# Kernel optimization log

Hardware: AMD Instinct MI355X
Metric: run time of the kernel (lower is better)

## Reference

```python
import jax, jax.numpy as jnp
import numpy as np

NUM_EMBEDDINGS = 8192
EMB_CHANNELS = 8
BETA = 0.25


def setup_inputs() -> dict:
    key = jax.random.key(0)
    k1, k2 = jax.random.split(key)
    z = jax.random.normal(k1, (8, EMB_CHANNELS, 64, 64), dtype=jnp.float32)
    # torch init: uniform(-1/K, 1/K)
    lim = 1.0 / NUM_EMBEDDINGS
    codebook = jax.random.uniform(
        k2, (NUM_EMBEDDINGS, EMB_CHANNELS), dtype=jnp.float32,
        minval=-lim, maxval=lim)
    return {"z": z, "codebook": codebook}


def reference(z, codebook):
    # z: [B, C, H, W]; codebook: [K, C]
    C = codebook.shape[1]
    z_ch = jnp.moveaxis(z, 1, -1)                 # [B, H, W, C]
    z_flat = z_ch.reshape(-1, C)                  # [N, C]
    # squared-euclidean distances via sum-of-squares + matmul: [N, K]
    dist = (
        jnp.sum(z_flat ** 2, axis=1, keepdims=True)
        + jnp.sum(codebook ** 2, axis=1)
        - 2.0 * jnp.einsum('nd,kd->nk', z_flat, codebook)
    )
    idx = jnp.argmin(dist, axis=1)                # [N]
    z_q = codebook[idx].reshape(z_ch.shape)       # [B, H, W, C]
    z_q = jnp.moveaxis(z_q, -1, 1)                # [B, C, H, W]
    sg = jax.lax.stop_gradient
    loss = (BETA * jnp.mean((sg(z_q) - z) ** 2)
            + jnp.mean((z_q - sg(z)) ** 2))
    # straight-through estimator
    z_q_st = z + sg(z_q - z)
    return z_q_st, loss
```

## Files before the change

kernel.cpp:

```cpp
#include <hip/hip_runtime.h>

typedef __attribute__((ext_vector_type(8))) short short8;
typedef __attribute__((ext_vector_type(4))) float f32x4;

#define NROWS 32768
#define NELEM 262144
#define KCB   8192

static __device__ __forceinline__ short to_bf16(float x) {
    unsigned u = __float_as_uint(x);
    unsigned r = (u + 0x7FFFu + ((u >> 16) & 1u)) >> 16;
    return (short)r;
}

__global__ __launch_bounds__(256) void vq_prep(
    const float* __restrict__ z, const float* __restrict__ cb,
    short8* __restrict__ cbb, short8* __restrict__ pka, float* __restrict__ out)
{
    int gid = blockIdx.x * 256 + threadIdx.x;
    if (gid == 0) out[NELEM] = 0.0f;
    if (gid < KCB) {
        const float4* p = (const float4*)(cb + (size_t)gid * 8);
        float4 a = p[0], b = p[1];
        float h = -0.5f * (a.x*a.x + a.y*a.y + a.z*a.z + a.w*a.w
                         + b.x*b.x + b.y*b.y + b.z*b.z + b.w*b.w);
        short8 lo = { to_bf16(a.x), to_bf16(a.y), to_bf16(a.z), to_bf16(a.w),
                      to_bf16(b.x), to_bf16(b.y), to_bf16(b.z), to_bf16(b.w) };
        short8 hi = { to_bf16(h), 0, 0, 0, 0, 0, 0, 0 };
        cbb[2 * gid]     = lo;
        cbb[2 * gid + 1] = hi;
    } else {
        int n = gid - KCB;
        int bb = n >> 12, hw = n & 4095;
        const float* zp = z + (size_t)bb * 32768 + hw;
        short8 v = { to_bf16(zp[0]),     to_bf16(zp[4096]),
                     to_bf16(zp[8192]),  to_bf16(zp[12288]),
                     to_bf16(zp[16384]), to_bf16(zp[20480]),
                     to_bf16(zp[24576]), to_bf16(zp[28672]) };
        pka[n] = v;
    }
}

__global__ __launch_bounds__(512, 4) void vq_main(
    const float* __restrict__ z, const float* __restrict__ cb,
    const short8* __restrict__ cbb, const short8* __restrict__ pka,
    float* __restrict__ out)
{
    __shared__ float sbest[8][64];
    __shared__ float lsum[8];

    const int tid  = threadIdx.x;
    const int lane = tid & 63;
    const int w    = tid >> 6;
    const int col  = lane & 15;
    const int g    = lane >> 4;

    const int row0 = blockIdx.x * 64;

    short8 af[4];
    #pragma unroll
    for (int f = 0; f < 4; ++f) {
        short8 v = {0, 0, 0, 0, 0, 0, 0, 0};
        if (g == 0)      v = pka[row0 + f * 16 + col];
        else if (g == 1) v[0] = (short)0x3F80;
        af[f] = v;
    }

    const int kbase = w * 1024;
    const char* bp = (const char*)cbb + (size_t)(kbase + col) * 32
                                      + (size_t)(g & 1) * 16;

    float best[4][4];
    #pragma unroll
    for (int f = 0; f < 4; ++f)
        #pragma unroll
        for (int r = 0; r < 4; ++r)
            best[f][r] = __uint_as_float(0xFF800000u);

    const unsigned inv0 = (unsigned)(8191 - (kbase + col));
    const f32x4 zacc = {0.f, 0.f, 0.f, 0.f};

    #pragma unroll 4
    for (int t = 0; t < 64; ++t) {
        short8 bf = *(const short8*)(bp + (size_t)t * 512);
        unsigned iv = inv0 - (unsigned)(t * 16);
        #pragma unroll
        for (int f = 0; f < 4; ++f) {
            f32x4 acc = __builtin_amdgcn_mfma_f32_16x16x32_bf16(af[f], bf, zacc, 0, 0, 0);
            #pragma unroll
            for (int r = 0; r < 4; ++r) {
                float p = __uint_as_float((__float_as_uint(acc[r]) & 0xFFFFE000u) | iv);
                best[f][r] = fmaxf(best[f][r], p);
            }
        }
    }

    #pragma unroll
    for (int d = 1; d < 16; d <<= 1)
        #pragma unroll
        for (int f = 0; f < 4; ++f)
            #pragma unroll
            for (int r = 0; r < 4; ++r)
                best[f][r] = fmaxf(best[f][r], __shfl_xor(best[f][r], d));

    if (col == 0) {
        #pragma unroll
        for (int f = 0; f < 4; ++f)
            #pragma unroll
            for (int r = 0; r < 4; ++r)
                sbest[w][f * 16 + g * 4 + r] = best[f][r];
    }
    __syncthreads();

    const int pos = tid & 63;
    const int ch  = tid >> 6;
    float m = sbest[0][pos];
    #pragma unroll
    for (int kw = 1; kw < 8; ++kw) m = fmaxf(m, sbest[kw][pos]);
    const int k = 8191 - (int)(__float_as_uint(m) & 8191u);

    const int n = row0 + pos;
    const size_t o = ((size_t)(n >> 12)) * 32768 + (size_t)ch * 4096 + (size_t)(n & 4095);
    float ev = cb[(size_t)k * 8 + ch];
    float zz = z[o];
    out[o] = ev;
    float dd = ev - zz;
    float sq = dd * dd;
    #pragma unroll
    for (int off = 32; off > 0; off >>= 1) sq += __shfl_down(sq, off);
    if (lane == 0) lsum[w] = sq;
    __syncthreads();
    if (tid == 0) {
        float s = lsum[0] + lsum[1] + lsum[2] + lsum[3]
                + lsum[4] + lsum[5] + lsum[6] + lsum[7];
        atomicAdd(out + NELEM, s * (1.25f / (float)NELEM));
    }
}

extern "C" void kernel_launch(void* const* d_in, const int* in_sizes, int n_in,
                              void* d_out, int out_size, void* d_ws, size_t ws_size,
                              hipStream_t stream)
{
    const float* z  = (const float*)d_in[0];
    const float* cb = (const float*)d_in[1];
    float* out = (float*)d_out;
    short8* cbb = (short8*)d_ws;
    short8* pka = (short8*)((char*)d_ws + 256 * 1024);

    vq_prep<<<(KCB + NROWS) / 256, 256, 0, stream>>>(z, cb, cbb, pka, out);
    vq_main<<<NROWS / 64, 512, 0, stream>>>(z, cb, cbb, pka, out);
}
```

Measured before the change: 33.61 us.

## Double rows per block with 16 waves and software-prefetch codebook tiles

Each block now handles 128 rows with 1024 threads (16 waves), and each wave covers 512 codebook entries instead of 1024. Every wave keeps 8 row fragments, so each loaded codebook tile feeds twice as many MFMAs, which halves total codebook reads. The inner loop is fully unrolled with explicit double-buffered prefetch of the next two tiles. In exchange, register pressure rises (8x4 best values plus 8 A fragments), and the grid halves to 256 blocks, which may reduce occupancy.

```diff
diff --git a/kernel.cpp b/kernel.cpp
--- a/kernel.cpp
+++ b/kernel.cpp
@@ -6,6 +6,8 @@
 #define NROWS 32768
 #define NELEM 262144
 #define KCB   8192
+#define ROWS_PB 128
+#define NWAVE 16
 
 static __device__ __forceinline__ short to_bf16(float x) {
     unsigned u = __float_as_uint(x);
@@ -41,13 +43,13 @@
     }
 }
 
-__global__ __launch_bounds__(512, 4) void vq_main(
+__global__ __launch_bounds__(1024, 4) void vq_main(
     const float* __restrict__ z, const float* __restrict__ cb,
     const short8* __restrict__ cbb, const short8* __restrict__ pka,
     float* __restrict__ out)
 {
-    __shared__ float sbest[8][64];
-    __shared__ float lsum[8];
+    __shared__ float sbest[NWAVE][ROWS_PB];
+    __shared__ float lsum[NWAVE];
 
     const int tid  = threadIdx.x;
     const int lane = tid & 63;
@@ -55,24 +57,24 @@
     const int col  = lane & 15;
     const int g    = lane >> 4;
 
-    const int row0 = blockIdx.x * 64;
+    const int row0 = blockIdx.x * ROWS_PB;
 
-    short8 af[4];
+    short8 af[8];
     #pragma unroll
-    for (int f = 0; f < 4; ++f) {
+    for (int f = 0; f < 8; ++f) {
         short8 v = {0, 0, 0, 0, 0, 0, 0, 0};
         if (g == 0)      v = pka[row0 + f * 16 + col];
         else if (g == 1) v[0] = (short)0x3F80;
         af[f] = v;
     }
 
-    const int kbase = w * 1024;
-    const char* bp = (const char*)cbb + (size_t)(kbase + col) * 32
-                                      + (size_t)(g & 1) * 16;
+    const int kbase = w * (KCB / NWAVE);
+    const char* bpc = (const char*)cbb + (size_t)(kbase + col) * 32
+                                       + (size_t)(g & 1) * 16;
 
-    float best[4][4];
+    float best[8][4];
     #pragma unroll
-    for (int f = 0; f < 4; ++f)
+    for (int f = 0; f < 8; ++f)
         #pragma unroll
         for (int r = 0; r < 4; ++r)
             best[f][r] = __uint_as_float(0xFF800000u);
@@ -80,12 +82,12 @@
     const unsigned inv0 = (unsigned)(8191 - (kbase + col));
     const f32x4 zacc = {0.f, 0.f, 0.f, 0.f};
 
-    #pragma unroll 4
-    for (int t = 0; t < 64; ++t) {
-        short8 bf = *(const short8*)(bp + (size_t)t * 512);
+#define LDT(T) (*(const short8*)(bpc + (size_t)(T) * 512))
+
+    auto comp = [&](short8 bf, int t) {
         unsigned iv = inv0 - (unsigned)(t * 16);
         #pragma unroll
-        for (int f = 0; f < 4; ++f) {
+        for (int f = 0; f < 8; ++f) {
             f32x4 acc = __builtin_amdgcn_mfma_f32_16x16x32_bf16(af[f], bf, zacc, 0, 0, 0);
             #pragma unroll
             for (int r = 0; r < 4; ++r) {
@@ -93,30 +95,41 @@
                 best[f][r] = fmaxf(best[f][r], p);
             }
         }
+    };
+
+    short8 c0 = LDT(0);
+    short8 c1 = LDT(1);
+    #pragma unroll
+    for (int tt = 0; tt < 16; ++tt) {
+        short8 n0, n1;
+        if (tt < 15) { n0 = LDT(2 * tt + 2); n1 = LDT(2 * tt + 3); }
+        comp(c0, 2 * tt);
+        comp(c1, 2 * tt + 1);
+        if (tt < 15) { c0 = n0; c1 = n1; }
     }
 
     #pragma unroll
     for (int d = 1; d < 16; d <<= 1)
         #pragma unroll
-        for (int f = 0; f < 4; ++f)
+        for (int f = 0; f < 8; ++f)
             #pragma unroll
             for (int r = 0; r < 4; ++r)
                 best[f][r] = fmaxf(best[f][r], __shfl_xor(best[f][r], d));
 
     if (col == 0) {
         #pragma unroll
-        for (int f = 0; f < 4; ++f)
+        for (int f = 0; f < 8; ++f)
             #pragma unroll
             for (int r = 0; r < 4; ++r)
                 sbest[w][f * 16 + g * 4 + r] = best[f][r];
     }
     __syncthreads();
 
-    const int pos = tid & 63;
-    const int ch  = tid >> 6;
+    const int pos = tid & 127;
+    const int ch  = tid >> 7;
     float m = sbest[0][pos];
     #pragma unroll
-    for (int kw = 1; kw < 8; ++kw) m = fmaxf(m, sbest[kw][pos]);
+    for (int kw = 1; kw < NWAVE; ++kw) m = fmaxf(m, sbest[kw][pos]);
     const int k = 8191 - (int)(__float_as_uint(m) & 8191u);
 
     const int n = row0 + pos;
@@ -131,8 +144,9 @@
     if (lane == 0) lsum[w] = sq;
     __syncthreads();
     if (tid == 0) {
-        float s = lsum[0] + lsum[1] + lsum[2] + lsum[3]
-                + lsum[4] + lsum[5] + lsum[6] + lsum[7];
+        float s = 0.f;
+        #pragma unroll
+        for (int kw = 0; kw < NWAVE; ++kw) s += lsum[kw];
         atomicAdd(out + NELEM, s * (1.25f / (float)NELEM));
     }
 }
@@ -148,5 +162,5 @@
     short8* pka = (short8*)((char*)d_ws + 256 * 1024);
 
     vq_prep<<<(KCB + NROWS) / 256, 256, 0, stream>>>(z, cb, cbb, pka, out);
-    vq_main<<<NROWS / 64, 512, 0, stream>>>(z, cb, cbb, pka, out);
+    vq_main<<<NROWS / ROWS_PB, 1024, 0, stream>>>(z, cb, cbb, pka, out);
 }
```

Result: slower. 39.48 us (+17.5%).

## Stream codebook tiles into per-wave LDS ring via async global_load_lds

Applied to the files above, without the earlier changes.

Replaces the direct per-iteration global loads of bf16 codebook fragments with a 4-deep per-wave LDS ring filled by global_load_lds, using vmcnt waits to overlap loading with MFMA work. Each step now processes two 16-code tiles, and the source addresses are XOR-swizzled to avoid LDS bank conflicts when reading fragments back. Launch bounds are raised to request 6 blocks per CU. This is meant to hide global memory latency in the distance loop, at the cost of extra LDS usage, LDS read traffic and more register pressure under the tighter occupancy target.

```diff
diff --git a/kernel.cpp b/kernel.cpp
--- a/kernel.cpp
+++ b/kernel.cpp
@@ -6,6 +6,8 @@
 #define NROWS 32768
 #define NELEM 262144
 #define KCB   8192
+#define ROWS_PB 64
+#define RING  4
 
 static __device__ __forceinline__ short to_bf16(float x) {
     unsigned u = __float_as_uint(x);
@@ -41,13 +43,16 @@
     }
 }
 
-__global__ __launch_bounds__(512, 4) void vq_main(
+#define WAITVM(n) asm volatile("s_waitcnt vmcnt(" #n ")" ::: "memory")
+
+__global__ __launch_bounds__(512, 6) void vq_main(
     const float* __restrict__ z, const float* __restrict__ cb,
     const short8* __restrict__ cbb, const short8* __restrict__ pka,
     float* __restrict__ out)
 {
-    __shared__ float sbest[8][64];
-    __shared__ float lsum[8];
+    __shared__ short8 ring[8][RING][64];
+    __shared__ float  sbest[8][ROWS_PB];
+    __shared__ float  lsum[8];
 
     const int tid  = threadIdx.x;
     const int lane = tid & 63;
@@ -55,7 +60,7 @@
     const int col  = lane & 15;
     const int g    = lane >> 4;
 
-    const int row0 = blockIdx.x * 64;
+    const int row0 = blockIdx.x * ROWS_PB;
 
     short8 af[4];
     #pragma unroll
@@ -67,8 +72,9 @@
     }
 
     const int kbase = w * 1024;
-    const char* bp = (const char*)cbb + (size_t)(kbase + col) * 32
-                                      + (size_t)(g & 1) * 16;
+    const char* cbbase = (const char*)cbb + (size_t)kbase * 32;
+    const unsigned srcswz = ((unsigned)lane * 16u) ^ (((unsigned)lane & 8u) << 1);
+    const int boff = col * 32 + (((g & 1) ^ ((col >> 2) & 1)) << 4);
 
     float best[4][4];
     #pragma unroll
@@ -80,20 +86,40 @@
     const unsigned inv0 = (unsigned)(8191 - (kbase + col));
     const f32x4 zacc = {0.f, 0.f, 0.f, 0.f};
 
-    #pragma unroll 4
-    for (int t = 0; t < 64; ++t) {
-        short8 bf = *(const short8*)(bp + (size_t)t * 512);
-        unsigned iv = inv0 - (unsigned)(t * 16);
+#define STAGE(p) __builtin_amdgcn_global_load_lds( \
+        (const __attribute__((address_space(1))) void*)(cbbase + (size_t)(p) * 1024 + srcswz), \
+        (__attribute__((address_space(3))) void*)&ring[w][(p) & 3][0], 16, 0, 0)
+
+    asm volatile("s_waitcnt vmcnt(0)" ::: "memory");
+    STAGE(0); STAGE(1); STAGE(2); STAGE(3);
+
+    auto comp2 = [&](const short8* base, unsigned iv0) {
+        short8 b0 = *(const short8*)((const char*)base + boff);
+        short8 b1 = *(const short8*)((const char*)base + boff + 512);
+        unsigned iv1 = iv0 - 16u;
         #pragma unroll
         for (int f = 0; f < 4; ++f) {
-            f32x4 acc = __builtin_amdgcn_mfma_f32_16x16x32_bf16(af[f], bf, zacc, 0, 0, 0);
+            f32x4 a0 = __builtin_amdgcn_mfma_f32_16x16x32_bf16(af[f], b0, zacc, 0, 0, 0);
+            f32x4 a1 = __builtin_amdgcn_mfma_f32_16x16x32_bf16(af[f], b1, zacc, 0, 0, 0);
             #pragma unroll
             for (int r = 0; r < 4; ++r) {
-                float p = __uint_as_float((__float_as_uint(acc[r]) & 0xFFFFE000u) | iv);
-                best[f][r] = fmaxf(best[f][r], p);
+                float p0 = __uint_as_float((__float_as_uint(a0[r]) & 0xFFFFE000u) | iv0);
+                float p1 = __uint_as_float((__float_as_uint(a1[r]) & 0xFFFFE000u) | iv1);
+                best[f][r] = fmaxf(fmaxf(p0, p1), best[f][r]);
             }
         }
+    };
+
+    #pragma unroll 4
+    for (int p = 0; p < 28; ++p) {
+        WAITVM(3);
+        comp2(&ring[w][p & 3][0], inv0 - (unsigned)(p * 32));
+        STAGE(p + 4);
     }
+    WAITVM(3); comp2(&ring[w][0][0], inv0 - 28u * 32u);
+    WAITVM(2); comp2(&ring[w][1][0], inv0 - 29u * 32u);
+    WAITVM(1); comp2(&ring[w][2][0], inv0 - 30u * 32u);
+    WAITVM(0); comp2(&ring[w][3][0], inv0 - 31u * 32u);
 
     #pragma unroll
     for (int d = 1; d < 16; d <<= 1)
@@ -131,8 +157,9 @@
     if (lane == 0) lsum[w] = sq;
     __syncthreads();
     if (tid == 0) {
-        float s = lsum[0] + lsum[1] + lsum[2] + lsum[3]
-                + lsum[4] + lsum[5] + lsum[6] + lsum[7];
+        float s = 0.f;
+        #pragma unroll
+        for (int kw = 0; kw < 8; ++kw) s += lsum[kw];
         atomicAdd(out + NELEM, s * (1.25f / (float)NELEM));
     }
 }
@@ -148,5 +175,5 @@
     short8* pka = (short8*)((char*)d_ws + 256 * 1024);
 
     vq_prep<<<(KCB + NROWS) / 256, 256, 0, stream>>>(z, cb, cbb, pka, out);
-    vq_main<<<NROWS / 64, 512, 0, stream>>>(z, cb, cbb, pka, out);
+    vq_main<<<NROWS / ROWS_PB, 512, 0, stream>>>(z, cb, cbb, pka, out);
 }
```

New measurement: 34.55 us. +2.8%, slower.

## Fuse z bf16 packing into main kernel, use 16 waves per block, software-prefetch codebook

Applied to the files above, without the earlier changes.

Drops the packed-z workspace pass in the prep kernel and instead converts z to bf16 directly while loading A fragments in the main kernel. The main kernel now uses 1024 threads (16 waves), each scanning 512 codes, which halves the serial MFMA loop per wave. The loop is reshaped to process two codebook tiles per iteration with loads prefetched one step ahead. The tradeoffs are strided z loads in the main kernel, half the threads idle in the epilogue, and higher register pressure from the 1024,8 launch bound.

```diff
diff --git a/kernel.cpp b/kernel.cpp
--- a/kernel.cpp
+++ b/kernel.cpp
@@ -6,6 +6,8 @@
 #define NROWS 32768
 #define NELEM 262144
 #define KCB   8192
+#define ROWS_PB 64
+#define NWAVE 16
 
 static __device__ __forceinline__ short to_bf16(float x) {
     unsigned u = __float_as_uint(x);
@@ -14,40 +16,27 @@
 }
 
 __global__ __launch_bounds__(256) void vq_prep(
-    const float* __restrict__ z, const float* __restrict__ cb,
-    short8* __restrict__ cbb, short8* __restrict__ pka, float* __restrict__ out)
+    const float* __restrict__ cb, short8* __restrict__ cbb, float* __restrict__ out)
 {
-    int gid = blockIdx.x * 256 + threadIdx.x;
-    if (gid == 0) out[NELEM] = 0.0f;
-    if (gid < KCB) {
-        const float4* p = (const float4*)(cb + (size_t)gid * 8);
-        float4 a = p[0], b = p[1];
-        float h = -0.5f * (a.x*a.x + a.y*a.y + a.z*a.z + a.w*a.w
-                         + b.x*b.x + b.y*b.y + b.z*b.z + b.w*b.w);
-        short8 lo = { to_bf16(a.x), to_bf16(a.y), to_bf16(a.z), to_bf16(a.w),
-                      to_bf16(b.x), to_bf16(b.y), to_bf16(b.z), to_bf16(b.w) };
-        short8 hi = { to_bf16(h), 0, 0, 0, 0, 0, 0, 0 };
-        cbb[2 * gid]     = lo;
-        cbb[2 * gid + 1] = hi;
-    } else {
-        int n = gid - KCB;
-        int bb = n >> 12, hw = n & 4095;
-        const float* zp = z + (size_t)bb * 32768 + hw;
-        short8 v = { to_bf16(zp[0]),     to_bf16(zp[4096]),
-                     to_bf16(zp[8192]),  to_bf16(zp[12288]),
-                     to_bf16(zp[16384]), to_bf16(zp[20480]),
-                     to_bf16(zp[24576]), to_bf16(zp[28672]) };
-        pka[n] = v;
-    }
+    int k = blockIdx.x * 256 + threadIdx.x;
+    if (k == 0) out[NELEM] = 0.0f;
+    const float4* p = (const float4*)(cb + (size_t)k * 8);
+    float4 a = p[0], b = p[1];
+    float h = -0.5f * (a.x*a.x + a.y*a.y + a.z*a.z + a.w*a.w
+                     + b.x*b.x + b.y*b.y + b.z*b.z + b.w*b.w);
+    short8 lo = { to_bf16(a.x), to_bf16(a.y), to_bf16(a.z), to_bf16(a.w),
+                  to_bf16(b.x), to_bf16(b.y), to_bf16(b.z), to_bf16(b.w) };
+    short8 hi = { to_bf16(h), 0, 0, 0, 0, 0, 0, 0 };
+    cbb[2 * k]     = lo;
+    cbb[2 * k + 1] = hi;
 }
 
-__global__ __launch_bounds__(512, 4) void vq_main(
+__global__ __launch_bounds__(1024, 8) void vq_main(
     const float* __restrict__ z, const float* __restrict__ cb,
-    const short8* __restrict__ cbb, const short8* __restrict__ pka,
-    float* __restrict__ out)
+    const short8* __restrict__ cbb, float* __restrict__ out)
 {
-    __shared__ float sbest[8][64];
-    __shared__ float lsum[8];
+    __shared__ float sbest[NWAVE][ROWS_PB];
+    __shared__ float lsum[NWAVE];
 
     const int tid  = threadIdx.x;
     const int lane = tid & 63;
@@ -55,20 +44,28 @@
     const int col  = lane & 15;
     const int g    = lane >> 4;
 
-    const int row0 = blockIdx.x * 64;
+    const int row0 = blockIdx.x * ROWS_PB;
 
     short8 af[4];
     #pragma unroll
     for (int f = 0; f < 4; ++f) {
         short8 v = {0, 0, 0, 0, 0, 0, 0, 0};
-        if (g == 0)      v = pka[row0 + f * 16 + col];
-        else if (g == 1) v[0] = (short)0x3F80;
+        if (g == 0) {
+            const int row = row0 + f * 16 + col;
+            const float* zp = z + (size_t)(row >> 12) * 32768 + (row & 4095);
+            v[0] = to_bf16(zp[0]);     v[1] = to_bf16(zp[4096]);
+            v[2] = to_bf16(zp[8192]);  v[3] = to_bf16(zp[12288]);
+            v[4] = to_bf16(zp[16384]); v[5] = to_bf16(zp[20480]);
+            v[6] = to_bf16(zp[24576]); v[7] = to_bf16(zp[28672]);
+        } else if (g == 1) {
+            v[0] = (short)0x3F80;
+        }
         af[f] = v;
     }
 
-    const int kbase = w * 1024;
-    const char* bp = (const char*)cbb + (size_t)(kbase + col) * 32
-                                      + (size_t)(g & 1) * 16;
+    const int kbase = w * (KCB / NWAVE);
+    const char* bpc = (const char*)cbb + (size_t)(kbase + col) * 32
+                                       + (size_t)(g & 1) * 16;
 
     float best[4][4];
     #pragma unroll
@@ -78,21 +75,34 @@
             best[f][r] = __uint_as_float(0xFF800000u);
 
     const unsigned inv0 = (unsigned)(8191 - (kbase + col));
+    const unsigned MSK = 0xFFFFE000u;
     const f32x4 zacc = {0.f, 0.f, 0.f, 0.f};
 
-    #pragma unroll 4
-    for (int t = 0; t < 64; ++t) {
-        short8 bf = *(const short8*)(bp + (size_t)t * 512);
-        unsigned iv = inv0 - (unsigned)(t * 16);
+#define LDT(T) (*(const short8*)(bpc + (size_t)(T) * 512))
+
+    auto comp2 = [&](short8 b0, short8 b1, unsigned iv0) {
+        const unsigned iv1 = iv0 - 16u;
         #pragma unroll
         for (int f = 0; f < 4; ++f) {
-            f32x4 acc = __builtin_amdgcn_mfma_f32_16x16x32_bf16(af[f], bf, zacc, 0, 0, 0);
+            f32x4 a0 = __builtin_amdgcn_mfma_f32_16x16x32_bf16(af[f], b0, zacc, 0, 0, 0);
+            f32x4 a1 = __builtin_amdgcn_mfma_f32_16x16x32_bf16(af[f], b1, zacc, 0, 0, 0);
             #pragma unroll
             for (int r = 0; r < 4; ++r) {
-                float p = __uint_as_float((__float_as_uint(acc[r]) & 0xFFFFE000u) | iv);
-                best[f][r] = fmaxf(best[f][r], p);
+                float p0 = __uint_as_float((__float_as_uint(a0[r]) & MSK) | iv0);
+                float p1 = __uint_as_float((__float_as_uint(a1[r]) & MSK) | iv1);
+                best[f][r] = fmaxf(fmaxf(p0, p1), best[f][r]);
             }
         }
+    };
+
+    short8 c0 = LDT(0);
+    short8 c1 = LDT(1);
+    #pragma unroll 4
+    for (int tt = 0; tt < 16; ++tt) {
+        short8 n0 = LDT((2 * tt + 2) & 31);
+        short8 n1 = LDT((2 * tt + 3) & 31);
+        comp2(c0, c1, inv0 - (unsigned)(tt * 32));
+        c0 = n0; c1 = n1;
     }
 
     #pragma unroll
@@ -112,27 +122,31 @@
     }
     __syncthreads();
 
-    const int pos = tid & 63;
-    const int ch  = tid >> 6;
-    float m = sbest[0][pos];
-    #pragma unroll
-    for (int kw = 1; kw < 8; ++kw) m = fmaxf(m, sbest[kw][pos]);
-    const int k = 8191 - (int)(__float_as_uint(m) & 8191u);
+    float sq = 0.0f;
+    if (tid < 512) {
+        const int pos = tid & 63;
+        const int ch  = tid >> 6;
+        float m = sbest[0][pos];
+        #pragma unroll
+        for (int kw = 1; kw < NWAVE; ++kw) m = fmaxf(m, sbest[kw][pos]);
+        const int k = 8191 - (int)(__float_as_uint(m) & 8191u);
 
-    const int n = row0 + pos;
-    const size_t o = ((size_t)(n >> 12)) * 32768 + (size_t)ch * 4096 + (size_t)(n & 4095);
-    float ev = cb[(size_t)k * 8 + ch];
-    float zz = z[o];
-    out[o] = ev;
-    float dd = ev - zz;
-    float sq = dd * dd;
+        const int n = row0 + pos;
+        const size_t o = ((size_t)(n >> 12)) * 32768 + (size_t)ch * 4096 + (size_t)(n & 4095);
+        float ev = cb[(size_t)k * 8 + ch];
+        float zz = z[o];
+        out[o] = ev;
+        float dd = ev - zz;
+        sq = dd * dd;
+    }
     #pragma unroll
     for (int off = 32; off > 0; off >>= 1) sq += __shfl_down(sq, off);
     if (lane == 0) lsum[w] = sq;
     __syncthreads();
     if (tid == 0) {
-        float s = lsum[0] + lsum[1] + lsum[2] + lsum[3]
-                + lsum[4] + lsum[5] + lsum[6] + lsum[7];
+        float s = 0.f;
+        #pragma unroll
+        for (int kw = 0; kw < NWAVE; ++kw) s += lsum[kw];
         atomicAdd(out + NELEM, s * (1.25f / (float)NELEM));
     }
 }
@@ -145,8 +159,7 @@
     const float* cb = (const float*)d_in[1];
     float* out = (float*)d_out;
     short8* cbb = (short8*)d_ws;
-    short8* pka = (short8*)((char*)d_ws + 256 * 1024);
 
-    vq_prep<<<(KCB + NROWS) / 256, 256, 0, stream>>>(z, cb, cbb, pka, out);
-    vq_main<<<NROWS / 64, 512, 0, stream>>>(z, cb, cbb, pka, out);
+    vq_prep<<<KCB / 256, 256, 0, stream>>>(cb, cbb, out);
+    vq_main<<<NROWS / ROWS_PB, 1024, 0, stream>>>(z, cb, cbb, out);
 }
```

New measurement: 46.01 us. +36.9%, slower.
